# Kernel optimization log

Hardware: AMD Instinct MI355X
Metric: run time of the kernel (lower is better)

The kernel has to match this reference:

```python
import jax, jax.numpy as jnp
import numpy as np

B, T, V = 64, 512, 32


def setup_inputs() -> dict:
    key = jax.random.key(0)
    k0, k1, k2, k3, k4, k5 = jax.random.split(key, 6)
    scores = jax.random.normal(k0, (B, T, V, V), dtype=jnp.float32)
    targets = jax.random.randint(k1, (B, T + 1), 0, V, dtype=jnp.int64)
    w_tx = jax.random.normal(k2, (V, V), dtype=jnp.float32) * 0.1
    w_init = jax.random.normal(k3, (V,), dtype=jnp.float32) * 0.1
    w_final = jax.random.normal(k4, (V,), dtype=jnp.float32) * 0.1
    w_dur = jax.random.normal(k5, (V, V), dtype=jnp.float32) * 0.1
    return {"scores": scores, "targets": targets, "w_tx": w_tx,
            "w_init": w_init, "w_final": w_final, "w_dur": w_dur}


def reference(scores, targets, w_tx, w_init, w_final, w_dur):
    """LatticeCrf.log_prob: per-sequence log p(y | x).

    Path score for states s_0..s_T:
      w_init[s_0] + w_final[s_T] + sum_t (scores[t, s_{t-1}, s_t] + w_tx + w_dur).
    Denominator is the CRF partition function via a forward scan over the
    [V,V] transition lattice (equivalent to obs o duration o transition FST
    composition followed by forward_score in the gtn original, with the
    default duration length D=1).
    """
    Bn, Tn, Vn, _ = scores.shape
    # per-frame combined arc weights: obs + transition + duration  [B,T,V,V]
    step = scores + (w_tx + w_dur)[None, None]

    def body(alpha, st):  # alpha [B,V], st [B,V,V]
        new = jax.nn.logsumexp(alpha[:, :, None] + st, axis=1)
        return new, None

    alpha0 = jnp.broadcast_to(w_init[None, :], (Bn, Vn))
    alphaT, _ = jax.lax.scan(body, alpha0, jnp.moveaxis(step, 1, 0))
    log_denom = jax.nn.logsumexp(alphaT + w_final[None, :], axis=-1)  # [B]

    src, dst = targets[:, :-1], targets[:, 1:]  # [B,T]
    b = jnp.arange(Bn)[:, None]
    t = jnp.arange(Tn)[None, :]
    log_num = (step[b, t, src, dst].sum(-1)
               + w_init[targets[:, 0]] + w_final[targets[:, -1]])  # [B]
    return log_num - log_denom
```

## Files before the change

kernel.cpp:

```cpp
#include <hip/hip_runtime.h>

#define BB 64
#define TT 512
#define VV 32
#define CC 8
#define LL (TT / CC)
#define MSTRIDE 40
#define SHIFT 6.0f
#define LOG2E 1.4426950408889634f
#define LN2f 0.6931471805599453f

__global__ __launch_bounds__(256) void crf_chunk_kernel(
    const float* __restrict__ scores,
    const float* __restrict__ w_tx,
    const float* __restrict__ w_dur,
    float* __restrict__ ws_M)
{
    __shared__ float Mlds[2][VV * MSTRIDE];
    __shared__ float Elds[VV * VV];

    const int tid = threadIdx.x;
    const int bc  = blockIdx.x;
    const int r   = tid >> 3;
    const int j0  = (tid & 7) * 4;

    const int widx = r * VV + j0;
    const float4 wtx4 = *(const float4*)(w_tx + widx);
    const float4 wdr4 = *(const float4*)(w_dur + widx);
    float4 w2;
    w2.x = (wtx4.x + wdr4.x) * LOG2E - SHIFT;
    w2.y = (wtx4.y + wdr4.y) * LOG2E - SHIFT;
    w2.z = (wtx4.z + wdr4.z) * LOG2E - SHIFT;
    w2.w = (wtx4.w + wdr4.w) * LOG2E - SHIFT;

    float4 id;
    id.x = (r == j0 + 0) ? 1.f : 0.f;
    id.y = (r == j0 + 1) ? 1.f : 0.f;
    id.z = (r == j0 + 2) ? 1.f : 0.f;
    id.w = (r == j0 + 3) ? 1.f : 0.f;
    *(float4*)&Mlds[0][r * MSTRIDE + j0] = id;

    const int b = bc >> 3, c = bc & 7;
    const float* sc = scores + ((size_t)b * TT + (size_t)c * LL) * (VV * VV);

    {
        float4 s = *(const float4*)(sc + tid * 4);
        float4 e;
        e.x = __builtin_amdgcn_exp2f(__builtin_fmaf(s.x, LOG2E, w2.x));
        e.y = __builtin_amdgcn_exp2f(__builtin_fmaf(s.y, LOG2E, w2.y));
        e.z = __builtin_amdgcn_exp2f(__builtin_fmaf(s.z, LOG2E, w2.z));
        e.w = __builtin_amdgcn_exp2f(__builtin_fmaf(s.w, LOG2E, w2.w));
        *(float4*)&Elds[tid * 4] = e;
    }
    __syncthreads();

    int p = 0;
    for (int t = 0; t < LL; ++t) {
        float4 snext;
        if (t + 1 < LL)
            snext = *(const float4*)(sc + (size_t)(t + 1) * (VV * VV) + tid * 4);

        float4 acc = make_float4(0.f, 0.f, 0.f, 0.f);
        const float* Mrow = &Mlds[p][r * MSTRIDE];
        #pragma unroll
        for (int i = 0; i < VV; ++i) {
            const float  m = Mrow[i];
            const float4 e = *(const float4*)&Elds[i * VV + j0];
            acc.x = __builtin_fmaf(m, e.x, acc.x);
            acc.y = __builtin_fmaf(m, e.y, acc.y);
            acc.z = __builtin_fmaf(m, e.z, acc.z);
            acc.w = __builtin_fmaf(m, e.w, acc.w);
        }
        *(float4*)&Mlds[1 - p][r * MSTRIDE + j0] = acc;
        __syncthreads();

        if (t + 1 < LL) {
            float4 e;
            e.x = __builtin_amdgcn_exp2f(__builtin_fmaf(snext.x, LOG2E, w2.x));
            e.y = __builtin_amdgcn_exp2f(__builtin_fmaf(snext.y, LOG2E, w2.y));
            e.z = __builtin_amdgcn_exp2f(__builtin_fmaf(snext.z, LOG2E, w2.z));
            e.w = __builtin_amdgcn_exp2f(__builtin_fmaf(snext.w, LOG2E, w2.w));
            *(float4*)&Elds[tid * 4] = e;
        }
        p ^= 1;
        __syncthreads();
    }

    float* outM = ws_M + (size_t)bc * (VV * VV);
    *(float4*)(outM + r * VV + j0) = *(float4*)&Mlds[p][r * MSTRIDE + j0];
}

__global__ __launch_bounds__(64) void crf_combine_kernel(
    const float* __restrict__ scores,
    const int*   __restrict__ targets,
    const float* __restrict__ w_tx,
    const float* __restrict__ w_init,
    const float* __restrict__ w_final,
    const float* __restrict__ w_dur,
    const float* __restrict__ ws_M,
    float* __restrict__ out)
{
    const int b    = blockIdx.x;
    const int lane = threadIdx.x;

    const int* tg = targets + b * (TT + 1);
    float num = 0.f;
    #pragma unroll
    for (int k = 0; k < TT / 64; ++k) {
        const int t  = lane + 64 * k;
        const int s_ = tg[t];
        const int d_ = tg[t + 1];
        const int wi = s_ * VV + d_;
        num += scores[(((size_t)b * TT + t) * VV + s_) * VV + d_] + w_tx[wi] + w_dur[wi];
    }
    #pragma unroll
    for (int m = 32; m >= 1; m >>= 1) num += __shfl_xor(num, m, 64);

    const int j = lane & 31;
    float a    = __builtin_amdgcn_exp2f(w_init[j] * LOG2E);
    float accl = 0.f;
    for (int c = 0; c < CC; ++c) {
        const float* M = ws_M + ((size_t)b * CC + c) * (VV * VV);
        float an = 0.f;
        #pragma unroll
        for (int i = 0; i < VV; ++i) {
            const float ai = __shfl(a, i, 32);
            an = __builtin_fmaf(ai, M[i * VV + j], an);
        }
        float mx = an;
        #pragma unroll
        for (int m = 16; m >= 1; m >>= 1) mx = fmaxf(mx, __shfl_xor(mx, m, 32));
        a = an / mx;
        accl += __builtin_amdgcn_logf(mx);
    }
    float rf = a * __builtin_amdgcn_exp2f(w_final[j] * LOG2E);
    float ss = rf;
    #pragma unroll
    for (int m = 16; m >= 1; m >>= 1) ss += __shfl_xor(ss, m, 32);
    const float denom_ln =
        (__builtin_amdgcn_logf(ss) + accl + SHIFT * (float)TT) * LN2f;

    if (lane == 0) {
        const float extra = w_init[tg[0]] + w_final[tg[TT]];
        out[b] = num + extra - denom_ln;
    }
}

extern "C" void kernel_launch(void* const* d_in, const int* in_sizes, int n_in,
                              void* d_out, int out_size, void* d_ws, size_t ws_size,
                              hipStream_t stream) {
    const float* scores  = (const float*)d_in[0];
    const int*   targets = (const int*)d_in[1];
    const float* w_tx    = (const float*)d_in[2];
    const float* w_init  = (const float*)d_in[3];
    const float* w_final = (const float*)d_in[4];
    const float* w_dur   = (const float*)d_in[5];
    float*       out     = (float*)d_out;
    float*       ws_M    = (float*)d_ws;

    crf_chunk_kernel<<<BB * CC, 256, 0, stream>>>(scores, w_tx, w_dur, ws_M);
    crf_combine_kernel<<<BB, 64, 0, stream>>>(scores, targets, w_tx, w_init,
                                              w_final, w_dur, ws_M, out);
}
```

Measured before the change: 233.2 us.

## Compute chunk transfer-matrix products with bf16 MFMA, one wavefront per chunk

The chunk kernel is rewritten so that each wavefront holds its running 32x32 product matrix in MFMA accumulator registers. Each step is two bf16 32x32x16 MFMA instructions, replacing the LDS-based fp32 FMA loop and its two block barriers per step. The launcher also picks more chunks (16 or 32) when the workspace allows, which raises parallelism and shortens the serial chain per chunk. The combine kernel prefetches the next chunk matrix into registers. Rounding the exponentiated scores and the accumulated products to bf16 at every step loses precision, and the error compounds over the sequence, which may push results outside tolerance.

New measurement: 234.6 us. About the same (+0.6%).

```diff
diff --git a/kernel.cpp b/kernel.cpp
--- a/kernel.cpp
+++ b/kernel.cpp
@@ -3,91 +3,103 @@
 #define BB 64
 #define TT 512
 #define VV 32
-#define CC 8
-#define LL (TT / CC)
-#define MSTRIDE 40
+#define LOG2E 1.4426950408889634f
+#define LN2f  0.6931471805599453f
 #define SHIFT 6.0f
-#define LOG2E 1.4426950408889634f
-#define LN2f 0.6931471805599453f
+
+typedef __bf16 bf16x8 __attribute__((ext_vector_type(8)));
+typedef float  f32x16 __attribute__((ext_vector_type(16)));
+
+union Frag { unsigned int u[4]; bf16x8 v; };
+
+__device__ __forceinline__ unsigned int pack_bf16(float lo, float hi) {
+    unsigned int a = __float_as_uint(lo) + 0x8000u;
+    unsigned int b = __float_as_uint(hi) + 0x8000u;
+    return __builtin_amdgcn_perm(b, a, 0x07060302u);
+}
 
 __global__ __launch_bounds__(256) void crf_chunk_kernel(
     const float* __restrict__ scores,
     const float* __restrict__ w_tx,
     const float* __restrict__ w_dur,
-    float* __restrict__ ws_M)
+    float* __restrict__ ws_M,
+    int CC, int L)
 {
-    __shared__ float Mlds[2][VV * MSTRIDE];
-    __shared__ float Elds[VV * VV];
-
-    const int tid = threadIdx.x;
-    const int bc  = blockIdx.x;
-    const int r   = tid >> 3;
-    const int j0  = (tid & 7) * 4;
-
-    const int widx = r * VV + j0;
-    const float4 wtx4 = *(const float4*)(w_tx + widx);
-    const float4 wdr4 = *(const float4*)(w_dur + widx);
-    float4 w2;
-    w2.x = (wtx4.x + wdr4.x) * LOG2E - SHIFT;
-    w2.y = (wtx4.y + wdr4.y) * LOG2E - SHIFT;
-    w2.z = (wtx4.z + wdr4.z) * LOG2E - SHIFT;
-    w2.w = (wtx4.w + wdr4.w) * LOG2E - SHIFT;
-
-    float4 id;
-    id.x = (r == j0 + 0) ? 1.f : 0.f;
-    id.y = (r == j0 + 1) ? 1.f : 0.f;
-    id.z = (r == j0 + 2) ? 1.f : 0.f;
-    id.w = (r == j0 + 3) ? 1.f : 0.f;
-    *(float4*)&Mlds[0][r * MSTRIDE + j0] = id;
-
-    const int b = bc >> 3, c = bc & 7;
-    const float* sc = scores + ((size_t)b * TT + (size_t)c * LL) * (VV * VV);
-
-    {
-        float4 s = *(const float4*)(sc + tid * 4);
-        float4 e;
-        e.x = __builtin_amdgcn_exp2f(__builtin_fmaf(s.x, LOG2E, w2.x));
-        e.y = __builtin_amdgcn_exp2f(__builtin_fmaf(s.y, LOG2E, w2.y));
-        e.z = __builtin_amdgcn_exp2f(__builtin_fmaf(s.z, LOG2E, w2.z));
-        e.w = __builtin_amdgcn_exp2f(__builtin_fmaf(s.w, LOG2E, w2.w));
-        *(float4*)&Elds[tid * 4] = e;
-    }
-    __syncthreads();
-
-    int p = 0;
-    for (int t = 0; t < LL; ++t) {
-        float4 snext;
-        if (t + 1 < LL)
-            snext = *(const float4*)(sc + (size_t)(t + 1) * (VV * VV) + tid * 4);
-
-        float4 acc = make_float4(0.f, 0.f, 0.f, 0.f);
-        const float* Mrow = &Mlds[p][r * MSTRIDE];
-        #pragma unroll
-        for (int i = 0; i < VV; ++i) {
-            const float  m = Mrow[i];
-            const float4 e = *(const float4*)&Elds[i * VV + j0];
-            acc.x = __builtin_fmaf(m, e.x, acc.x);
-            acc.y = __builtin_fmaf(m, e.y, acc.y);
-            acc.z = __builtin_fmaf(m, e.z, acc.z);
-            acc.w = __builtin_fmaf(m, e.w, acc.w);
-        }
-        *(float4*)&Mlds[1 - p][r * MSTRIDE + j0] = acc;
-        __syncthreads();
-
-        if (t + 1 < LL) {
-            float4 e;
-            e.x = __builtin_amdgcn_exp2f(__builtin_fmaf(snext.x, LOG2E, w2.x));
-            e.y = __builtin_amdgcn_exp2f(__builtin_fmaf(snext.y, LOG2E, w2.y));
-            e.z = __builtin_amdgcn_exp2f(__builtin_fmaf(snext.z, LOG2E, w2.z));
-            e.w = __builtin_amdgcn_exp2f(__builtin_fmaf(snext.w, LOG2E, w2.w));
-            *(float4*)&Elds[tid * 4] = e;
-        }
-        p ^= 1;
-        __syncthreads();
-    }
-
-    float* outM = ws_M + (size_t)bc * (VV * VV);
-    *(float4*)(outM + r * VV + j0) = *(float4*)&Mlds[p][r * MSTRIDE + j0];
+    const int lane = threadIdx.x & 63;
+    const int wid  = threadIdx.x >> 6;
+    const int chunk = blockIdx.x * 4 + wid;
+    const int m = lane & 31;
+    const int h = lane >> 5;
+
+    const int base = h * 128 + m;
+
+    float w2[16];
+#pragma unroll
+    for (int j = 0; j < 8; ++j) {
+        const int off = base + (j & 3) * 32 + (j >> 2) * 256;
+        w2[j]     = (w_tx[off]       + w_dur[off])       * LOG2E - SHIFT;
+        w2[j + 8] = (w_tx[off + 512] + w_dur[off + 512]) * LOG2E - SHIFT;
+    }
+
+    const int b = chunk / CC, c = chunk - b * CC;
+    const float* sc = scores + ((size_t)(b * TT + c * L)) * 1024 + base;
+
+    float s[16];
+#pragma unroll
+    for (int j = 0; j < 8; ++j) {
+        const int off = (j & 3) * 32 + (j >> 2) * 256;
+        s[j]     = sc[off];
+        s[j + 8] = sc[off + 512];
+    }
+
+    f32x16 acc;
+#pragma unroll
+    for (int r = 0; r < 16; ++r) {
+        const int mr = (r & 3) + 8 * (r >> 2) + 4 * h;
+        acc[r] = (mr == m) ? 1.0f : 0.0f;
+    }
+
+    for (int t = 0; t < L; ++t) {
+        float fa[16];
+#pragma unroll
+        for (int j = 0; j < 16; ++j) fa[j] = __builtin_fmaf(s[j], LOG2E, w2[j]);
+
+        if (t + 1 < L) {
+            const float* sn = sc + (size_t)(t + 1) * 1024;
+#pragma unroll
+            for (int j = 0; j < 8; ++j) {
+                const int off = (j & 3) * 32 + (j >> 2) * 256;
+                s[j]     = sn[off];
+                s[j + 8] = sn[off + 512];
+            }
+        }
+
+        float e[16];
+#pragma unroll
+        for (int j = 0; j < 16; ++j) e[j] = __builtin_amdgcn_exp2f(fa[j]);
+
+        Frag a1, a2, b1, b2;
+#pragma unroll
+        for (int p = 0; p < 4; ++p) {
+            a1.u[p] = pack_bf16(e[2 * p],        e[2 * p + 1]);
+            a2.u[p] = pack_bf16(e[8 + 2 * p],    e[8 + 2 * p + 1]);
+            b1.u[p] = pack_bf16(acc[2 * p],      acc[2 * p + 1]);
+            b2.u[p] = pack_bf16(acc[8 + 2 * p],  acc[8 + 2 * p + 1]);
+        }
+
+        f32x16 z;
+#pragma unroll
+        for (int r = 0; r < 16; ++r) z[r] = 0.0f;
+        f32x16 tmp = __builtin_amdgcn_mfma_f32_32x32x16_bf16(a1.v, b1.v, z,   0, 0, 0);
+        acc        = __builtin_amdgcn_mfma_f32_32x32x16_bf16(a2.v, b2.v, tmp, 0, 0, 0);
+    }
+
+    float* outP = ws_M + (size_t)chunk * 1024;
+#pragma unroll
+    for (int r = 0; r < 16; ++r) {
+        const int mr = (r & 3) + 8 * (r >> 2) + 4 * h;
+        outP[mr * 32 + m] = acc[r];
+    }
 }
 
 __global__ __launch_bounds__(64) void crf_combine_kernel(
@@ -98,14 +110,15 @@
     const float* __restrict__ w_final,
     const float* __restrict__ w_dur,
     const float* __restrict__ ws_M,
-    float* __restrict__ out)
+    float* __restrict__ out,
+    int CC)
 {
     const int b    = blockIdx.x;
     const int lane = threadIdx.x;
 
     const int* tg = targets + b * (TT + 1);
     float num = 0.f;
-    #pragma unroll
+#pragma unroll
     for (int k = 0; k < TT / 64; ++k) {
         const int t  = lane + 64 * k;
         const int s_ = tg[t];
@@ -113,36 +126,54 @@
         const int wi = s_ * VV + d_;
         num += scores[(((size_t)b * TT + t) * VV + s_) * VV + d_] + w_tx[wi] + w_dur[wi];
     }
-    #pragma unroll
-    for (int m = 32; m >= 1; m >>= 1) num += __shfl_xor(num, m, 64);
+#pragma unroll
+    for (int mS = 32; mS >= 1; mS >>= 1) num += __shfl_xor(num, mS, 64);
 
     const int j = lane & 31;
     float a    = __builtin_amdgcn_exp2f(w_init[j] * LOG2E);
     float accl = 0.f;
+    const float* Pb = ws_M + (size_t)b * CC * 1024;
+
+    float4 rr[8];
+#pragma unroll
+    for (int q = 0; q < 8; ++q) rr[q] = *(const float4*)(Pb + j * 32 + 4 * q);
+
     for (int c = 0; c < CC; ++c) {
-        const float* M = ws_M + ((size_t)b * CC + c) * (VV * VV);
+        float4 rn[8];
+        if (c + 1 < CC) {
+            const float* Pn = Pb + (size_t)(c + 1) * 1024 + j * 32;
+#pragma unroll
+            for (int q = 0; q < 8; ++q) rn[q] = *(const float4*)(Pn + 4 * q);
+        }
         float an = 0.f;
-        #pragma unroll
-        for (int i = 0; i < VV; ++i) {
-            const float ai = __shfl(a, i, 32);
-            an = __builtin_fmaf(ai, M[i * VV + j], an);
+#pragma unroll
+        for (int i = 0; i < 32; ++i) {
+            const float  ai = __shfl(a, i, 32);
+            const float4 v  = rr[i >> 2];
+            const float  pv = ((i & 3) == 0) ? v.x : ((i & 3) == 1) ? v.y
+                             : ((i & 3) == 2) ? v.z : v.w;
+            an = __builtin_fmaf(ai, pv, an);
         }
         float mx = an;
-        #pragma unroll
-        for (int m = 16; m >= 1; m >>= 1) mx = fmaxf(mx, __shfl_xor(mx, m, 32));
+#pragma unroll
+        for (int mS = 16; mS >= 1; mS >>= 1) mx = fmaxf(mx, __shfl_xor(mx, mS, 32));
         a = an / mx;
         accl += __builtin_amdgcn_logf(mx);
-    }
+        if (c + 1 < CC) {
+#pragma unroll
+            for (int q = 0; q < 8; ++q) rr[q] = rn[q];
+        }
+    }
+
     float rf = a * __builtin_amdgcn_exp2f(w_final[j] * LOG2E);
     float ss = rf;
-    #pragma unroll
-    for (int m = 16; m >= 1; m >>= 1) ss += __shfl_xor(ss, m, 32);
+#pragma unroll
+    for (int mS = 16; mS >= 1; mS >>= 1) ss += __shfl_xor(ss, mS, 32);
     const float denom_ln =
         (__builtin_amdgcn_logf(ss) + accl + SHIFT * (float)TT) * LN2f;
 
     if (lane == 0) {
-        const float extra = w_init[tg[0]] + w_final[tg[TT]];
-        out[b] = num + extra - denom_ln;
+        out[b] = num + w_init[tg[0]] + w_final[tg[TT]] - denom_ln;
     }
 }
 
@@ -158,7 +189,12 @@
     float*       out     = (float*)d_out;
     float*       ws_M    = (float*)d_ws;
 
-    crf_chunk_kernel<<<BB * CC, 256, 0, stream>>>(scores, w_tx, w_dur, ws_M);
+    int CC = 8;
+    if      (ws_size >= (size_t)BB * 32 * 4096) CC = 32;
+    else if (ws_size >= (size_t)BB * 16 * 4096) CC = 16;
+    const int L = TT / CC;
+
+    crf_chunk_kernel<<<BB * CC / 4, 256, 0, stream>>>(scores, w_tx, w_dur, ws_M, CC, L);
     crf_combine_kernel<<<BB, 64, 0, stream>>>(scores, targets, w_tx, w_init,
-                                              w_final, w_dur, ws_M, out);
-}
+                                              w_final, w_dur, ws_M, out, CC);
+}
```
